# Optimization experiments

Measured on AMD Instinct MI355X. Metric: run time of the kernel, lower is better.

## Reference

```python
import jax, jax.numpy as jnp
import numpy as np


def setup_inputs() -> dict:
    key = jax.random.key(0)
    ks = jax.random.split(key, 8)
    B, H, W, C = 4, 64, 64, 64
    Cf = C // 8
    x = jax.random.normal(ks[0], (B, H, W, C), dtype=jnp.float32)
    # 1x1 conv kernels stored as [C_in, C_out] (kernel_size=1)
    w_f = jax.random.normal(ks[1], (C, Cf), dtype=jnp.float32) * 0.05
    b_f = jax.random.normal(ks[2], (Cf,), dtype=jnp.float32) * 0.05
    w_g = jax.random.normal(ks[3], (C, Cf), dtype=jnp.float32) * 0.05
    b_g = jax.random.normal(ks[4], (Cf,), dtype=jnp.float32) * 0.05
    w_h = jax.random.normal(ks[5], (C, C), dtype=jnp.float32) * 0.05
    b_h = jax.random.normal(ks[6], (C,), dtype=jnp.float32) * 0.05
    gamma = jax.random.normal(ks[7], (1,), dtype=jnp.float32) * 0.1
    return {"x": x, "w_f": w_f, "b_f": b_f, "w_g": w_g, "b_g": b_g,
            "w_h": w_h, "b_h": b_h, "gamma": gamma}


def reference(x, w_f, b_f, w_g, b_g, w_h, b_h, gamma):
    B, H, W, C = x.shape
    N = H * W
    xf = x.reshape(B, N, C)  # 1x1 conv == per-pixel linear
    f = xf @ w_f + b_f       # [B, N, C/8]
    g = xf @ w_g + b_g       # [B, N, C/8]
    h = xf @ w_h + b_h       # [B, N, C]
    # attention_map[b, i, j] = <g_i, f_j>, softmax over last axis
    scores = jnp.einsum('bic,bjc->bij', g, f)  # [B, N, N]
    attn = jax.nn.softmax(scores, axis=-1)
    out = jnp.einsum('bij,bjc->bic', attn, h)  # [B, N, C]
    out = out.reshape(B, H, W, C)
    return gamma * out + x
```

## Files before the change

### kernel.cpp

```cpp
#include <hip/hip_runtime.h>
#include <hip/hip_bf16.h>

typedef __bf16 bf16;
typedef __bf16 bf16x8 __attribute__((ext_vector_type(8)));
typedef __bf16 bf16x4 __attribute__((ext_vector_type(4)));
typedef float floatx4 __attribute__((ext_vector_type(4)));

#define NPIX 4096
#define BATCH 4

__device__ inline bf16x8 zero8() {
    bf16x8 v;
    #pragma unroll
    for (int i = 0; i < 8; ++i) v[i] = (bf16)0.0f;
    return v;
}

__global__ __launch_bounds__(256) void proj_kernel(
    const float* __restrict__ x,
    const float* __restrict__ w_f, const float* __restrict__ b_f,
    const float* __restrict__ w_g, const float* __restrict__ b_g,
    const float* __restrict__ w_h, const float* __restrict__ b_h,
    bf16* __restrict__ fq, bf16* __restrict__ gq, bf16* __restrict__ hT)
{
    __shared__ bf16 xs[64 * 72];
    __shared__ bf16 wt[80 * 72];
    __shared__ float bs[80];
    const int tid = threadIdx.x;
    const int p0 = blockIdx.x * 64;

    {
        const float4* xg = (const float4*)(x + (long)p0 * 64);
        #pragma unroll
        for (int it = 0; it < 4; ++it) {
            int i4 = tid + it * 256;
            float4 v = xg[i4];
            int row = i4 >> 4, c4 = (i4 & 15) * 4;
            bf16x4 pk;
            pk[0] = (bf16)v.x; pk[1] = (bf16)v.y; pk[2] = (bf16)v.z; pk[3] = (bf16)v.w;
            *(bf16x4*)(&xs[row * 72 + c4]) = pk;
        }
    }
    for (int idx = tid; idx < 80 * 64; idx += 256) {
        int n = idx >> 6, c = idx & 63;
        float v = (n < 8) ? w_f[c * 8 + n]
                : (n < 16) ? w_g[c * 8 + (n - 8)]
                : w_h[c * 64 + (n - 16)];
        wt[n * 72 + c] = (bf16)v;
    }
    if (tid < 80)
        bs[tid] = (tid < 8) ? b_f[tid] : (tid < 16) ? b_g[tid - 8] : b_h[tid - 16];
    __syncthreads();

    const int wv = tid >> 6, lane = tid & 63;
    const int quad = lane >> 4, l15 = lane & 15;
    const int b = blockIdx.x >> 6;
    const int n0pix = (p0 & (NPIX - 1)) + wv * 16 + quad * 4;

    bf16x8 a0 = *(const bf16x8*)(&xs[(wv * 16 + l15) * 72 + quad * 8]);
    bf16x8 a1 = *(const bf16x8*)(&xs[(wv * 16 + l15) * 72 + 32 + quad * 8]);

    #pragma unroll
    for (int nt = 0; nt < 5; ++nt) {
        float bias = bs[nt * 16 + l15];
        floatx4 acc = {bias, bias, bias, bias};
        bf16x8 b0 = *(const bf16x8*)(&wt[(nt * 16 + l15) * 72 + quad * 8]);
        bf16x8 b1 = *(const bf16x8*)(&wt[(nt * 16 + l15) * 72 + 32 + quad * 8]);
        acc = __builtin_amdgcn_mfma_f32_16x16x32_bf16(a0, b0, acc, 0, 0, 0);
        acc = __builtin_amdgcn_mfma_f32_16x16x32_bf16(a1, b1, acc, 0, 0, 0);
        if (nt == 0) {
            #pragma unroll
            for (int r = 0; r < 4; ++r) {
                long P = (long)p0 + wv * 16 + quad * 4 + r;
                bf16 v = (bf16)acc[r];
                if (l15 < 8) fq[P * 8 + l15] = v;
                else         gq[P * 8 + (l15 - 8)] = v;
            }
        } else {
            int c = nt * 16 + l15 - 16;
            bf16x4 pk;
            pk[0] = (bf16)acc[0]; pk[1] = (bf16)acc[1];
            pk[2] = (bf16)acc[2]; pk[3] = (bf16)acc[3];
            *(bf16x4*)(&hT[((long)b * 64 + c) * NPIX + n0pix]) = pk;
        }
    }
}

#define LDSF(h, buf) (((h) * 2 + (buf)) * 2048)
#define LDSH(h, buf) (8192 + ((h) * 2 + (buf)) * 17408)
#define LDSP(w)      (77824 + (w) * 4352)
#define LDSDEN       112640
#define LDSTOT       113152

__global__ __launch_bounds__(512) void attn_kernel(
    const bf16* __restrict__ fq, const bf16* __restrict__ gq,
    const bf16* __restrict__ hT, const float* __restrict__ x,
    const float* __restrict__ gamma_p, float* __restrict__ out)
{
    __shared__ char smem[LDSTOT];
    const int tid  = threadIdx.x;
    const int wv   = tid >> 6, lane = tid & 63;
    const int quad = lane >> 4, l15 = lane & 15;
    const int grp  = wv & 3, half = wv >> 2;
    const int b    = blockIdx.x >> 6, it = blockIdx.x & 63;
    const long rowbase = (long)b * NPIX + it * 64 + grp * 16;
    const float sgamma = gamma_p[0];

    bf16x8 gfrag = zero8();
    if (lane < 16) gfrag = *(const bf16x8*)(gq + (rowbase + lane) * 8);

    const char* gPtr[9]; int ldsOff[9], ldsDlt[9], gStep[9];
    #pragma unroll
    for (int k = 0; k < 9; ++k) {
        int ch = k * 512 + tid;
        int h  = (ch >= 2304) ? 1 : 0;
        int c2 = ch - h * 2304;
        if (c2 < 256) {
            ldsOff[k] = LDSF(h, 0) + c2 * 8;
            ldsDlt[k] = 2048;
            gPtr[k]   = (const char*)fq + (long)(b * NPIX + h * 2048) * 16 + c2 * 8;
            gStep[k]  = 128 * 16;
        } else {
            int q = c2 - 256, c = q >> 5, j8 = q & 31;
            ldsOff[k] = LDSH(h, 0) + c * 272 + j8 * 8;
            ldsDlt[k] = 17408;
            gPtr[k]   = (const char*)hT + ((long)b * 64 + c) * (NPIX * 2)
                        + h * 2048 * 2 + j8 * 8;
            gStep[k]  = 128 * 2;
        }
    }

    floatx4 acc[4];
    #pragma unroll
    for (int nt = 0; nt < 4; ++nt) acc[nt] = (floatx4){0.f, 0.f, 0.f, 0.f};
    float denp = 0.f;
    bf16* Pw = (bf16*)(smem + LDSP(wv));

    #pragma unroll
    for (int k = 0; k < 9; ++k) {
        *(float2*)(smem + ldsOff[k]) = *(const float2*)gPtr[k];
        gPtr[k] += gStep[k];
    }
    __syncthreads();

    for (int t = 0; t < 16; ++t) {
        const int buf = t & 1;
        float2 pre[9];
        if (t < 15) {
            #pragma unroll
            for (int k = 0; k < 9; ++k) {
                pre[k] = *(const float2*)gPtr[k];
                gPtr[k] += gStep[k];
            }
        }
        const bf16* Fb = (const bf16*)(smem + LDSF(half, buf));
        const bf16* Hb = (const bf16*)(smem + LDSH(half, buf));

        #pragma unroll
        for (int js = 0; js < 8; ++js) {
            bf16x8 afrag = zero8();
            if (lane < 16) afrag = *(const bf16x8*)(Fb + (js * 16 + l15) * 8);
            floatx4 s = __builtin_amdgcn_mfma_f32_16x16x32_bf16(
                afrag, gfrag, (floatx4){0.f, 0.f, 0.f, 0.f}, 0, 0, 0);
            float e0 = __expf(s[0]), e1 = __expf(s[1]);
            float e2 = __expf(s[2]), e3 = __expf(s[3]);
            denp += (e0 + e1) + (e2 + e3);
            bf16x4 pk;
            pk[0] = (bf16)e0; pk[1] = (bf16)e1; pk[2] = (bf16)e2; pk[3] = (bf16)e3;
            *(bf16x4*)(Pw + l15 * 136 + js * 16 + quad * 4) = pk;
        }
        #pragma unroll
        for (int ks = 0; ks < 4; ++ks) {
            bf16x8 pfrag = *(const bf16x8*)(Pw + l15 * 136 + ks * 32 + quad * 8);
            #pragma unroll
            for (int nt = 0; nt < 4; ++nt) {
                bf16x8 bfrag = *(const bf16x8*)(Hb + (nt * 16 + l15) * 136 + ks * 32 + quad * 8);
                acc[nt] = __builtin_amdgcn_mfma_f32_16x16x32_bf16(pfrag, bfrag, acc[nt], 0, 0, 0);
            }
        }
        __syncthreads();
        if (t < 15) {
            #pragma unroll
            for (int k = 0; k < 9; ++k)
                *(float2*)(smem + ldsOff[k] + (buf ^ 1) * ldsDlt[k]) = pre[k];
        }
        __syncthreads();
    }

    denp += __shfl_xor(denp, 16);
    denp += __shfl_xor(denp, 32);

    float* red  = (float*)(smem + (long)grp * 4352);
    float* denr = (float*)(smem + LDSDEN);
    if (lane < 16) denr[half * 64 + grp * 16 + l15] = denp;
    if (half == 0) {
        #pragma unroll
        for (int nt = 0; nt < 4; ++nt)
            #pragma unroll
            for (int r = 0; r < 4; ++r)
                red[(quad * 4 + r) * 68 + nt * 16 + l15] = acc[nt][r];
    }
    __syncthreads();
    if (half == 1) {
        float rden[4];
        #pragma unroll
        for (int r = 0; r < 4; ++r) {
            int i = grp * 16 + quad * 4 + r;
            rden[r] = 1.0f / (denr[i] + denr[64 + i]);
        }
        #pragma unroll
        for (int nt = 0; nt < 4; ++nt) {
            #pragma unroll
            for (int r = 0; r < 4; ++r) {
                float num = acc[nt][r] + red[(quad * 4 + r) * 68 + nt * 16 + l15];
                long off = (rowbase + quad * 4 + r) * 64 + nt * 16 + l15;
                out[off] = sgamma * (num * rden[r]) + x[off];
            }
        }
    }
}

extern "C" void kernel_launch(void* const* d_in, const int* in_sizes, int n_in,
                              void* d_out, int out_size, void* d_ws, size_t ws_size,
                              hipStream_t stream) {
    const float* x     = (const float*)d_in[0];
    const float* w_f   = (const float*)d_in[1];
    const float* b_f   = (const float*)d_in[2];
    const float* w_g   = (const float*)d_in[3];
    const float* b_g   = (const float*)d_in[4];
    const float* w_h   = (const float*)d_in[5];
    const float* b_h   = (const float*)d_in[6];
    const float* gamma = (const float*)d_in[7];
    float* out = (float*)d_out;

    bf16* fq = (bf16*)d_ws;
    bf16* gq = fq + 16384 * 8;
    bf16* hT = gq + 16384 * 8;

    proj_kernel<<<256, 256, 0, stream>>>(x, w_f, b_f, w_g, b_g, w_h, b_h, fq, gq, hT);
    attn_kernel<<<256, 512, 0, stream>>>(fq, gq, hT, x, gamma, out);
}
```

Measured before the change: 107.1 us.

## Switch P·V attention product to FP8 MFMA and halve rows per block

The h projection is now stored as FP8 (e4m3) instead of bf16, the unnormalized softmax numerators are packed to FP8, and the second attention GEMM uses the fp8 MFMA, halving LDS and global traffic for h and P. The attention kernel is reorganized to 256 threads per block handling 32 query rows, with 512 blocks and a much smaller LDS footprint, so more blocks can be resident per CU. FP8 rounding of exp scores (which are unnormalized and can be large) and of h reduces accuracy and risks exceeding tolerance.

New measurement: 106.2 us. No clear change (-0.8%).

```diff
diff --git a/kernel.cpp b/kernel.cpp
--- a/kernel.cpp
+++ b/kernel.cpp
@@ -5,6 +5,10 @@
 typedef __bf16 bf16x8 __attribute__((ext_vector_type(8)));
 typedef __bf16 bf16x4 __attribute__((ext_vector_type(4)));
 typedef float floatx4 __attribute__((ext_vector_type(4)));
+
+typedef int    aint    __attribute__((may_alias));
+typedef long   along   __attribute__((may_alias));
+typedef float2 afloat2 __attribute__((may_alias));
 
 #define NPIX 4096
 #define BATCH 4
@@ -21,7 +25,7 @@
     const float* __restrict__ w_f, const float* __restrict__ b_f,
     const float* __restrict__ w_g, const float* __restrict__ b_g,
     const float* __restrict__ w_h, const float* __restrict__ b_h,
-    bf16* __restrict__ fq, bf16* __restrict__ gq, bf16* __restrict__ hT)
+    bf16* __restrict__ fq, bf16* __restrict__ gq, unsigned char* __restrict__ hT)
 {
     __shared__ bf16 xs[64 * 72];
     __shared__ bf16 wt[80 * 72];
@@ -78,55 +82,54 @@
             }
         } else {
             int c = nt * 16 + l15 - 16;
-            bf16x4 pk;
-            pk[0] = (bf16)acc[0]; pk[1] = (bf16)acc[1];
-            pk[2] = (bf16)acc[2]; pk[3] = (bf16)acc[3];
-            *(bf16x4*)(&hT[((long)b * 64 + c) * NPIX + n0pix]) = pk;
-        }
-    }
-}
-
-#define LDSF(h, buf) (((h) * 2 + (buf)) * 2048)
-#define LDSH(h, buf) (8192 + ((h) * 2 + (buf)) * 17408)
-#define LDSP(w)      (77824 + (w) * 4352)
-#define LDSDEN       112640
-#define LDSTOT       113152
-
-__global__ __launch_bounds__(512) void attn_kernel(
+            int pk = __builtin_amdgcn_cvt_pk_fp8_f32(acc[0], acc[1], 0, false);
+            pk     = __builtin_amdgcn_cvt_pk_fp8_f32(acc[2], acc[3], pk, true);
+            *(aint*)(hT + ((long)b * 64 + c) * NPIX + n0pix) = pk;
+        }
+    }
+}
+
+#define FBASE 0
+#define HBASE 8192
+#define PBASE 45056
+#define DENBASE 54272
+#define LDSTOT 54528
+
+__global__ __launch_bounds__(256) void attn_kernel(
     const bf16* __restrict__ fq, const bf16* __restrict__ gq,
-    const bf16* __restrict__ hT, const float* __restrict__ x,
+    const unsigned char* __restrict__ hT, const float* __restrict__ x,
     const float* __restrict__ gamma_p, float* __restrict__ out)
 {
     __shared__ char smem[LDSTOT];
     const int tid  = threadIdx.x;
     const int wv   = tid >> 6, lane = tid & 63;
     const int quad = lane >> 4, l15 = lane & 15;
-    const int grp  = wv & 3, half = wv >> 2;
-    const int b    = blockIdx.x >> 6, it = blockIdx.x & 63;
-    const long rowbase = (long)b * NPIX + it * 64 + grp * 16;
+    const int grp  = wv & 1, half = wv >> 1;
+    const int b    = blockIdx.x >> 7, it = blockIdx.x & 127;
+    const long rowbase = (long)b * NPIX + it * 32 + grp * 16;
     const float sgamma = gamma_p[0];
 
     bf16x8 gfrag = zero8();
     if (lane < 16) gfrag = *(const bf16x8*)(gq + (rowbase + lane) * 8);
 
-    const char* gPtr[9]; int ldsOff[9], ldsDlt[9], gStep[9];
-    #pragma unroll
-    for (int k = 0; k < 9; ++k) {
-        int ch = k * 512 + tid;
-        int h  = (ch >= 2304) ? 1 : 0;
-        int c2 = ch - h * 2304;
-        if (c2 < 256) {
-            ldsOff[k] = LDSF(h, 0) + c2 * 8;
+    const char* gPtr[10]; int ldsOff[10], ldsDlt[10], gStep[10];
+    #pragma unroll
+    for (int k = 0; k < 10; ++k) {
+        int ch = k * 256 + tid;
+        if (ch < 512) {
+            int h = ch >> 8, c2 = ch & 255;
+            ldsOff[k] = FBASE + h * 2 * 2048 + c2 * 8;
             ldsDlt[k] = 2048;
             gPtr[k]   = (const char*)fq + (long)(b * NPIX + h * 2048) * 16 + c2 * 8;
             gStep[k]  = 128 * 16;
         } else {
-            int q = c2 - 256, c = q >> 5, j8 = q & 31;
-            ldsOff[k] = LDSH(h, 0) + c * 272 + j8 * 8;
-            ldsDlt[k] = 17408;
-            gPtr[k]   = (const char*)hT + ((long)b * 64 + c) * (NPIX * 2)
-                        + h * 2048 * 2 + j8 * 8;
-            gStep[k]  = 128 * 2;
+            int q = ch - 512;
+            int h = q >> 10, r = q & 1023, c = r >> 4, j8 = r & 15;
+            ldsOff[k] = HBASE + h * 2 * 9216 + c * 144 + j8 * 8;
+            ldsDlt[k] = 9216;
+            gPtr[k]   = (const char*)hT + ((long)b * 64 + c) * NPIX
+                        + h * 2048 + j8 * 8;
+            gStep[k]  = 128;
         }
     }
 
@@ -134,55 +137,56 @@
     #pragma unroll
     for (int nt = 0; nt < 4; ++nt) acc[nt] = (floatx4){0.f, 0.f, 0.f, 0.f};
     float denp = 0.f;
-    bf16* Pw = (bf16*)(smem + LDSP(wv));
-
-    #pragma unroll
-    for (int k = 0; k < 9; ++k) {
-        *(float2*)(smem + ldsOff[k]) = *(const float2*)gPtr[k];
+    char* Pw = smem + PBASE + wv * 2304;
+
+    #pragma unroll
+    for (int k = 0; k < 10; ++k) {
+        *(afloat2*)(smem + ldsOff[k]) = *(const float2*)gPtr[k];
         gPtr[k] += gStep[k];
     }
     __syncthreads();
 
     for (int t = 0; t < 16; ++t) {
         const int buf = t & 1;
-        float2 pre[9];
+        float2 pre[10];
         if (t < 15) {
             #pragma unroll
-            for (int k = 0; k < 9; ++k) {
+            for (int k = 0; k < 10; ++k) {
                 pre[k] = *(const float2*)gPtr[k];
                 gPtr[k] += gStep[k];
             }
         }
-        const bf16* Fb = (const bf16*)(smem + LDSF(half, buf));
-        const bf16* Hb = (const bf16*)(smem + LDSH(half, buf));
+        const char* Fb = smem + FBASE + (half * 2 + buf) * 2048;
+        const char* Hb = smem + HBASE + (half * 2 + buf) * 9216;
 
         #pragma unroll
         for (int js = 0; js < 8; ++js) {
             bf16x8 afrag = zero8();
-            if (lane < 16) afrag = *(const bf16x8*)(Fb + (js * 16 + l15) * 8);
+            if (lane < 16) afrag = *(const bf16x8*)(Fb + (js * 16 + l15) * 16);
             floatx4 s = __builtin_amdgcn_mfma_f32_16x16x32_bf16(
                 afrag, gfrag, (floatx4){0.f, 0.f, 0.f, 0.f}, 0, 0, 0);
             float e0 = __expf(s[0]), e1 = __expf(s[1]);
             float e2 = __expf(s[2]), e3 = __expf(s[3]);
             denp += (e0 + e1) + (e2 + e3);
-            bf16x4 pk;
-            pk[0] = (bf16)e0; pk[1] = (bf16)e1; pk[2] = (bf16)e2; pk[3] = (bf16)e3;
-            *(bf16x4*)(Pw + l15 * 136 + js * 16 + quad * 4) = pk;
-        }
+            int pk = __builtin_amdgcn_cvt_pk_fp8_f32(e0, e1, 0, false);
+            pk     = __builtin_amdgcn_cvt_pk_fp8_f32(e2, e3, pk, true);
+            *(aint*)(Pw + l15 * 144 + js * 16 + quad * 4) = pk;
+        }
+        asm volatile("" ::: "memory");
         #pragma unroll
         for (int ks = 0; ks < 4; ++ks) {
-            bf16x8 pfrag = *(const bf16x8*)(Pw + l15 * 136 + ks * 32 + quad * 8);
+            along pfrag = *(const along*)(Pw + l15 * 144 + ks * 32 + quad * 8);
             #pragma unroll
             for (int nt = 0; nt < 4; ++nt) {
-                bf16x8 bfrag = *(const bf16x8*)(Hb + (nt * 16 + l15) * 136 + ks * 32 + quad * 8);
-                acc[nt] = __builtin_amdgcn_mfma_f32_16x16x32_bf16(pfrag, bfrag, acc[nt], 0, 0, 0);
+                along bfrag = *(const along*)(Hb + (nt * 16 + l15) * 144 + ks * 32 + quad * 8);
+                acc[nt] = __builtin_amdgcn_mfma_f32_16x16x32_fp8_fp8(pfrag, bfrag, acc[nt], 0, 0, 0);
             }
         }
         __syncthreads();
         if (t < 15) {
             #pragma unroll
-            for (int k = 0; k < 9; ++k)
-                *(float2*)(smem + ldsOff[k] + (buf ^ 1) * ldsDlt[k]) = pre[k];
+            for (int k = 0; k < 10; ++k)
+                *(afloat2*)(smem + ldsOff[k] + (buf ^ 1) * ldsDlt[k]) = pre[k];
         }
         __syncthreads();
     }
@@ -190,15 +194,15 @@
     denp += __shfl_xor(denp, 16);
     denp += __shfl_xor(denp, 32);
 
-    float* red  = (float*)(smem + (long)grp * 4352);
-    float* denr = (float*)(smem + LDSDEN);
-    if (lane < 16) denr[half * 64 + grp * 16 + l15] = denp;
+    float* denr = (float*)(smem + DENBASE);
+    float* red  = (float*)smem;
+    if (lane < 16) denr[half * 32 + grp * 16 + l15] = denp;
     if (half == 0) {
         #pragma unroll
         for (int nt = 0; nt < 4; ++nt)
             #pragma unroll
             for (int r = 0; r < 4; ++r)
-                red[(quad * 4 + r) * 68 + nt * 16 + l15] = acc[nt][r];
+                red[grp * 1088 + (quad * 4 + r) * 68 + nt * 16 + l15] = acc[nt][r];
     }
     __syncthreads();
     if (half == 1) {
@@ -206,13 +210,13 @@
         #pragma unroll
         for (int r = 0; r < 4; ++r) {
             int i = grp * 16 + quad * 4 + r;
-            rden[r] = 1.0f / (denr[i] + denr[64 + i]);
+            rden[r] = 1.0f / (denr[i] + denr[32 + i]);
         }
         #pragma unroll
         for (int nt = 0; nt < 4; ++nt) {
             #pragma unroll
             for (int r = 0; r < 4; ++r) {
-                float num = acc[nt][r] + red[(quad * 4 + r) * 68 + nt * 16 + l15];
+                float num = acc[nt][r] + red[grp * 1088 + (quad * 4 + r) * 68 + nt * 16 + l15];
                 long off = (rowbase + quad * 4 + r) * 64 + nt * 16 + l15;
                 out[off] = sgamma * (num * rden[r]) + x[off];
             }
@@ -235,8 +239,8 @@
 
     bf16* fq = (bf16*)d_ws;
     bf16* gq = fq + 16384 * 8;
-    bf16* hT = gq + 16384 * 8;
+    unsigned char* hT = (unsigned char*)(gq + 16384 * 8);
 
     proj_kernel<<<256, 256, 0, stream>>>(x, w_f, b_f, w_g, b_g, w_h, b_h, fq, gq, hT);
-    attn_kernel<<<256, 512, 0, stream>>>(fq, gq, hT, x, gamma, out);
-}
+    attn_kernel<<<512, 256, 0, stream>>>(fq, gq, hT, x, gamma, out);
+}
```
